# Kernel tuning notes

Hardware: AMD Instinct MI355X
Metric: run time of the kernel (lower is better)

Reference implementation:

```python
import jax, jax.numpy as jnp
import numpy as np

BOUND = 2.0
MIN_NEAR = 0.05
N_RAYS = 131072   # 512x256 image worth of rays
N_COARSE = 128    # coarse intervals -> bins has N_COARSE+1 edges


def setup_inputs() -> dict:
    key = jax.random.key(0)
    k1, k2, k3 = jax.random.split(key, 3)
    rays_o = jax.random.normal(k1, (N_RAYS, 3), jnp.float32) * 0.5  # origins inside the bound cube
    rays_d = jax.random.normal(k2, (N_RAYS, 3), jnp.float32)
    rays_d = rays_d / jnp.linalg.norm(rays_d, axis=-1, keepdims=True)  # unit directions
    weights = jax.random.uniform(k3, (N_RAYS, N_COARSE), jnp.float32)  # coarse-pass weights
    return {"rays_o": rays_o, "rays_d": rays_d, "weights": weights, "n_importance": 128}


def _near_far_cube(rays_o, rays_d, bound, min_near):
    # AABB slab test, identical to near_far_from_bound(type='cube')
    tmin = (-bound - rays_o) / (rays_d + 1e-15)   # [N,3]
    tmax = (bound - rays_o) / (rays_d + 1e-15)
    near = jnp.max(jnp.minimum(tmin, tmax), axis=-1, keepdims=True)  # [N,1]
    far = jnp.min(jnp.maximum(tmin, tmax), axis=-1, keepdims=True)
    miss = far < near
    near = jnp.where(miss, 1e9, near)
    far = jnp.where(miss, 1e9, far)
    near = jnp.maximum(near, min_near)
    return near, far


def _sample_pdf(bins, weights, n_samples):
    # Inverse-CDF importance sampling (det=True), identical math to sample_pdf.
    weights = weights + 1e-5
    pdf = weights / jnp.sum(weights, axis=-1, keepdims=True)           # [N,T]
    cdf = jnp.cumsum(pdf, axis=-1)
    cdf = jnp.concatenate([jnp.zeros_like(cdf[..., :1]), cdf], axis=-1)  # [N,T+1]
    C = cdf.shape[-1]
    u = jnp.linspace(0.5 / n_samples, 1.0 - 0.5 / n_samples, n_samples, dtype=cdf.dtype)
    u = jnp.broadcast_to(u, cdf.shape[:-1] + (n_samples,))              # [N,S]
    inds = jax.vmap(lambda c, uu: jnp.searchsorted(c, uu, side='right'))(cdf, u)
    below = jnp.maximum(inds - 1, 0)
    above = jnp.minimum(inds, C - 1)
    cdf_b = jnp.take_along_axis(cdf, below, axis=-1)    # [N,S]
    cdf_a = jnp.take_along_axis(cdf, above, axis=-1)
    bins_b = jnp.take_along_axis(bins, below, axis=-1)
    bins_a = jnp.take_along_axis(bins, above, axis=-1)
    denom = cdf_a - cdf_b
    denom = jnp.where(denom < 1e-5, jnp.ones_like(denom), denom)
    t = (u - cdf_b) / denom
    return bins_b + t * (bins_a - bins_b)               # [N,S]


def reference(rays_o, rays_d, weights, n_importance):
    near, far = _near_far_cube(rays_o, rays_d, BOUND, MIN_NEAR)
    # uniform coarse bin edges between near and far (as in the renderer's run())
    t = jnp.linspace(0.0, 1.0, weights.shape[-1] + 1, dtype=rays_o.dtype)
    bins = near + (far - near) * t[None, :]             # [N, T+1]
    return _sample_pdf(bins, weights, n_importance)     # [N, n_importance]
```

## Files before the change

### kernel.cpp

```cpp
#include <hip/hip_runtime.h>

#define BOUNDV 2.0f
#define MIN_NEAR 0.05f
#define TCOARSE 128
#define NIMP 128
#define INV128 0.0078125f
#define INV256 0.00390625f

__device__ __forceinline__ float scan16(float S) {
    int m;
    m = __builtin_amdgcn_update_dpp(0, __float_as_int(S), 0x111, 0xf, 0xf, true);
    S += __int_as_float(m);
    m = __builtin_amdgcn_update_dpp(0, __float_as_int(S), 0x112, 0xf, 0xf, true);
    S += __int_as_float(m);
    m = __builtin_amdgcn_update_dpp(0, __float_as_int(S), 0x114, 0xf, 0xf, true);
    S += __int_as_float(m);
    m = __builtin_amdgcn_update_dpp(0, __float_as_int(S), 0x118, 0xf, 0xf, true);
    S += __int_as_float(m);
    return S;
}

__global__ __launch_bounds__(256) void nerf_sample_pdf_kernel(
    const float* __restrict__ rays_o,
    const float* __restrict__ rays_d,
    const float* __restrict__ weights,
    float* __restrict__ out,
    int n_rays)
{
    __shared__ float stg[4][512];

    const int tid  = threadIdx.x;
    const int lane = tid & 63;
    const int wv   = tid >> 6;
    const int grp  = (tid >> 4) & 3;
    const int l16  = tid & 15;
    const int ray  = blockIdx.x * 16 + (tid >> 4);

    if (ray < n_rays) {
        const float* ro = rays_o + (size_t)ray * 3;
        const float* rd = rays_d + (size_t)ray * 3;
        float o0 = ro[0], o1 = ro[1], o2 = ro[2];
        float e0 = rd[0], e1 = rd[1], e2 = rd[2];

        const float* wp = weights + (size_t)ray * TCOARSE + 8 * l16;
        float4 wa = *reinterpret_cast<const float4*>(wp);
        float4 wb = *reinterpret_cast<const float4*>(wp + 4);

        float nr = -1e30f, fr = 1e30f;
        {
            float o[3] = {o0, o1, o2};
            float e[3] = {e0, e1, e2};
            #pragma unroll
            for (int c = 0; c < 3; ++c) {
                float dd = e[c] + 1e-15f;
                float r  = __builtin_amdgcn_rcpf(dd);
                float t0 = (-BOUNDV - o[c]) * r;
                float t1 = ( BOUNDV - o[c]) * r;
                nr = fmaxf(nr, fminf(t0, t1));
                fr = fminf(fr, fmaxf(t0, t1));
            }
        }
        if (fr < nr) { nr = 1e9f; fr = 1e9f; }
        nr = fmaxf(nr, MIN_NEAR);
        float near = nr;
        float bw   = (fr - nr) * INV128;

        float w[8], q[8], invw[8];
        w[0] = wa.x + 1e-5f; w[1] = wa.y + 1e-5f;
        w[2] = wa.z + 1e-5f; w[3] = wa.w + 1e-5f;
        w[4] = wb.x + 1e-5f; w[5] = wb.y + 1e-5f;
        w[6] = wb.z + 1e-5f; w[7] = wb.w + 1e-5f;
        q[0] = w[0];
        #pragma unroll
        for (int j = 1; j < 8; ++j) q[j] = q[j - 1] + w[j];
        #pragma unroll
        for (int j = 0; j < 8; ++j) invw[j] = __builtin_amdgcn_rcpf(w[j]);

        float S    = scan16(q[7]);
        float excl = __int_as_float(__builtin_amdgcn_update_dpp(
            0, __float_as_int(S), 0x111, 0xf, 0xf, true));
        float total = __int_as_float(
            __builtin_amdgcn_ds_swizzle(__float_as_int(S), 0x1F0));
        float it   = __builtin_amdgcn_rcpf(total);
        float s128 = 128.0f * it;
        float t128 = INV128 * total;
        float t256 = INV256 * total;
        float thr  = 1e-5f * total;
        float slr  = bw * it;

        float sl[8];
        #pragma unroll
        for (int j = 0; j < 8; ++j)
            sl[j] = (w[j] < thr) ? slr : bw * invw[j];

        float* srow = &stg[wv][grp * 128];
        float bb = fmaf(bw, (float)(8 * l16), near);

        float p_prev   = excl;
        float knf_prev = ceilf(fmaf(excl, s128, -0.5f));
        int   k_prev   = (int)knf_prev;

        #pragma unroll
        for (int j = 0; j < 8; ++j) {
            float pj  = (j == 7) ? S : (excl + q[j]);
            float knf = ceilf(fmaf(pj, s128, -0.5f));
            int   kn  = (int)knf;
            int   cnt = kn - k_prev;
            float u1   = fmaf(knf_prev, t128, t256);
            float step = t128 * sl[j];
            float v1   = fmaf(u1 - p_prev, sl[j], bb);
            float* pk  = srow + k_prev;
            if (cnt > 0) pk[0] = v1;
            if (cnt > 1) pk[1] = v1 + step;
            if (cnt > 2) pk[2] = fmaf(2.0f, step, v1);
            if (cnt > 3) pk[3] = fmaf(3.0f, step, v1);
            p_prev = pj; k_prev = kn; knf_prev = knf; bb += bw;
        }
    }

    __builtin_amdgcn_wave_barrier();

    int wbase = blockIdx.x * 16 + wv * 4;
    if (wbase + 4 <= n_rays) {
        const float4* sf = reinterpret_cast<const float4*>(&stg[wv][0]);
        float4 v0 = sf[lane];
        float4 v1 = sf[64 + lane];
        float4* ob4 = reinterpret_cast<float4*>(out + (size_t)wbase * NIMP);
        ob4[lane]      = v0;
        ob4[64 + lane] = v1;
    } else if (wbase < n_rays) {
        const float4* sf = reinterpret_cast<const float4*>(&stg[wv][0]);
        float4* ob4 = reinterpret_cast<float4*>(out + (size_t)wbase * NIMP);
        int rays_left = n_rays - wbase;
        if (lane < rays_left * 32)      ob4[lane]      = sf[lane];
        if (64 + lane < rays_left * 32) ob4[64 + lane] = sf[64 + lane];
    }
}

extern "C" void kernel_launch(void* const* d_in, const int* in_sizes, int n_in,
                              void* d_out, int out_size, void* d_ws, size_t ws_size,
                              hipStream_t stream) {
    const float* rays_o  = (const float*)d_in[0];
    const float* rays_d  = (const float*)d_in[1];
    const float* weights = (const float*)d_in[2];
    float* out = (float*)d_out;

    int n_rays = in_sizes[0] / 3;
    int blocks = (n_rays + 15) / 16;
    hipLaunchKernelGGL(nerf_sample_pdf_kernel, dim3(blocks), dim3(256), 0, stream,
                       rays_o, rays_d, weights, out, n_rays);
}
```

Before: 25.77 us.

## Process four ray batches per wave with double-buffered register prefetch

Each wave now handles 16 rays in four batches of 4 instead of a single batch, and the grid shrinks by a factor of four. Loads for the next batch are issued into a second register set before the current batch is computed and flushed, so memory latency overlaps with compute. The cost is fewer blocks, which means less latency hiding through occupancy across the GPU, plus extra registers to hold two ray batches. Wave barriers around each LDS-staged flush keep the shared staging buffer from being overwritten early.

```diff
diff --git a/kernel.cpp b/kernel.cpp
--- a/kernel.cpp
+++ b/kernel.cpp
@@ -20,6 +20,118 @@
     return S;
 }
 
+struct RayRegs {
+    float o0, o1, o2, e0, e1, e2;
+    float4 wa, wb;
+};
+
+__device__ __forceinline__ void issue_loads(const float* __restrict__ rays_o,
+                                            const float* __restrict__ rays_d,
+                                            const float* __restrict__ weights,
+                                            int ray, int l16, bool valid, RayRegs& R)
+{
+    if (!valid) return;
+    const float* ro = rays_o + (size_t)ray * 3;
+    const float* rd = rays_d + (size_t)ray * 3;
+    R.o0 = ro[0]; R.o1 = ro[1]; R.o2 = ro[2];
+    R.e0 = rd[0]; R.e1 = rd[1]; R.e2 = rd[2];
+    const float* wp = weights + (size_t)ray * TCOARSE + 8 * l16;
+    R.wa = *reinterpret_cast<const float4*>(wp);
+    R.wb = *reinterpret_cast<const float4*>(wp + 4);
+}
+
+__device__ __forceinline__ void compute_scatter(const RayRegs& R, int l16,
+                                                float* __restrict__ srow)
+{
+    float nr = -1e30f, fr = 1e30f;
+    {
+        float o[3] = {R.o0, R.o1, R.o2};
+        float e[3] = {R.e0, R.e1, R.e2};
+        #pragma unroll
+        for (int c = 0; c < 3; ++c) {
+            float dd = e[c] + 1e-15f;
+            float r  = __builtin_amdgcn_rcpf(dd);
+            float t0 = (-BOUNDV - o[c]) * r;
+            float t1 = ( BOUNDV - o[c]) * r;
+            nr = fmaxf(nr, fminf(t0, t1));
+            fr = fminf(fr, fmaxf(t0, t1));
+        }
+    }
+    if (fr < nr) { nr = 1e9f; fr = 1e9f; }
+    nr = fmaxf(nr, MIN_NEAR);
+    float near = nr;
+    float bw   = (fr - nr) * INV128;
+
+    float w[8], q[8], sl[8];
+    w[0] = R.wa.x + 1e-5f; w[1] = R.wa.y + 1e-5f;
+    w[2] = R.wa.z + 1e-5f; w[3] = R.wa.w + 1e-5f;
+    w[4] = R.wb.x + 1e-5f; w[5] = R.wb.y + 1e-5f;
+    w[6] = R.wb.z + 1e-5f; w[7] = R.wb.w + 1e-5f;
+    q[0] = w[0];
+    #pragma unroll
+    for (int j = 1; j < 8; ++j) q[j] = q[j - 1] + w[j];
+    #pragma unroll
+    for (int j = 0; j < 8; ++j) sl[j] = __builtin_amdgcn_rcpf(w[j]);
+
+    float S    = scan16(q[7]);
+    float excl = __int_as_float(__builtin_amdgcn_update_dpp(
+        0, __float_as_int(S), 0x111, 0xf, 0xf, true));
+    float total = __int_as_float(
+        __builtin_amdgcn_ds_swizzle(__float_as_int(S), 0x1F0));
+    float it   = __builtin_amdgcn_rcpf(total);
+    float s128 = 128.0f * it;
+    float t128 = INV128 * total;
+    float t256 = INV256 * total;
+    float thr  = 1e-5f * total;
+    float slr  = bw * it;
+
+    #pragma unroll
+    for (int j = 0; j < 8; ++j)
+        sl[j] = (w[j] < thr) ? slr : bw * sl[j];
+
+    float bb = fmaf(bw, (float)(8 * l16), near);
+    float p_prev   = excl;
+    float knf_prev = ceilf(fmaf(excl, s128, -0.5f));
+    int   k_prev   = (int)knf_prev;
+
+    #pragma unroll
+    for (int j = 0; j < 8; ++j) {
+        float pj  = (j == 7) ? S : (excl + q[j]);
+        float knf = ceilf(fmaf(pj, s128, -0.5f));
+        int   kn  = (int)knf;
+        int   cnt = kn - k_prev;
+        float u1   = fmaf(knf_prev, t128, t256);
+        float step = t128 * sl[j];
+        float v1   = fmaf(u1 - p_prev, sl[j], bb);
+        float* pk  = srow + k_prev;
+        if (cnt > 0) pk[0] = v1;
+        if (cnt > 1) pk[1] = v1 + step;
+        if (cnt > 2) pk[2] = fmaf(2.0f, step, v1);
+        if (cnt > 3) pk[3] = fmaf(3.0f, step, v1);
+        p_prev = pj; k_prev = kn; knf_prev = knf; bb += bw;
+    }
+}
+
+__device__ __forceinline__ void flush_batch(const float* __restrict__ stgw,
+                                            float* __restrict__ out,
+                                            int wbase, int lane, int n_rays)
+{
+    __builtin_amdgcn_wave_barrier();
+    const float4* sf = reinterpret_cast<const float4*>(stgw);
+    float4* ob4 = reinterpret_cast<float4*>(out + (size_t)wbase * NIMP);
+    if (wbase + 4 <= n_rays) {
+        float4 v0 = sf[lane];
+        float4 v1 = sf[64 + lane];
+        ob4[lane]      = v0;
+        ob4[64 + lane] = v1;
+    } else if (wbase < n_rays) {
+        int rays_left = n_rays - wbase;
+        if (lane < rays_left * 32)      ob4[lane]      = sf[lane];
+        if (64 + lane < rays_left * 32) ob4[64 + lane] = sf[64 + lane];
+    }
+    __builtin_amdgcn_wave_barrier();
+}
+
 __global__ __launch_bounds__(256) void nerf_sample_pdf_kernel(
     const float* __restrict__ rays_o,
     const float* __restrict__ rays_d,
@@ -34,107 +146,33 @@
     const int wv   = tid >> 6;
     const int grp  = (tid >> 4) & 3;
     const int l16  = tid & 15;
-    const int ray  = blockIdx.x * 16 + (tid >> 4);
 
-    if (ray < n_rays) {
-        const float* ro = rays_o + (size_t)ray * 3;
-        const float* rd = rays_d + (size_t)ray * 3;
-        float o0 = ro[0], o1 = ro[1], o2 = ro[2];
-        float e0 = rd[0], e1 = rd[1], e2 = rd[2];
+    const int wbase = (blockIdx.x * 4 + wv) * 16;
+    const int r0 = wbase + grp;
+    const int r1 = wbase + 4 + grp;
+    const int r2 = wbase + 8 + grp;
+    const int r3 = wbase + 12 + grp;
 
-        const float* wp = weights + (size_t)ray * TCOARSE + 8 * l16;
-        float4 wa = *reinterpret_cast<const float4*>(wp);
-        float4 wb = *reinterpret_cast<const float4*>(wp + 4);
+    float* srow = &stg[wv][grp * 128];
+    float* stgw = &stg[wv][0];
 
-        float nr = -1e30f, fr = 1e30f;
-        {
-            float o[3] = {o0, o1, o2};
-            float e[3] = {e0, e1, e2};
-            #pragma unroll
-            for (int c = 0; c < 3; ++c) {
-                float dd = e[c] + 1e-15f;
-                float r  = __builtin_amdgcn_rcpf(dd);
-                float t0 = (-BOUNDV - o[c]) * r;
-                float t1 = ( BOUNDV - o[c]) * r;
-                nr = fmaxf(nr, fminf(t0, t1));
-                fr = fminf(fr, fmaxf(t0, t1));
-            }
-        }
-        if (fr < nr) { nr = 1e9f; fr = 1e9f; }
-        nr = fmaxf(nr, MIN_NEAR);
-        float near = nr;
-        float bw   = (fr - nr) * INV128;
+    RayRegs A, B;
+    issue_loads(rays_o, rays_d, weights, r0, l16, r0 < n_rays, A);
+    issue_loads(rays_o, rays_d, weights, r1, l16, r1 < n_rays, B);
 
-        float w[8], q[8], invw[8];
-        w[0] = wa.x + 1e-5f; w[1] = wa.y + 1e-5f;
-        w[2] = wa.z + 1e-5f; w[3] = wa.w + 1e-5f;
-        w[4] = wb.x + 1e-5f; w[5] = wb.y + 1e-5f;
-        w[6] = wb.z + 1e-5f; w[7] = wb.w + 1e-5f;
-        q[0] = w[0];
-        #pragma unroll
-        for (int j = 1; j < 8; ++j) q[j] = q[j - 1] + w[j];
-        #pragma unroll
-        for (int j = 0; j < 8; ++j) invw[j] = __builtin_amdgcn_rcpf(w[j]);
+    if (r0 < n_rays) compute_scatter(A, l16, srow);
+    issue_loads(rays_o, rays_d, weights, r2, l16, r2 < n_rays, A);
+    flush_batch(stgw, out, wbase, lane, n_rays);
 
-        float S    = scan16(q[7]);
-        float excl = __int_as_float(__builtin_amdgcn_update_dpp(
-            0, __float_as_int(S), 0x111, 0xf, 0xf, true));
-        float total = __int_as_float(
-            __builtin_amdgcn_ds_swizzle(__float_as_int(S), 0x1F0));
-        float it   = __builtin_amdgcn_rcpf(total);
-        float s128 = 128.0f * it;
-        float t128 = INV128 * total;
-        float t256 = INV256 * total;
-        float thr  = 1e-5f * total;
-        float slr  = bw * it;
+    if (r1 < n_rays) compute_scatter(B, l16, srow);
+    issue_loads(rays_o, rays_d, weights, r3, l16, r3 < n_rays, B);
+    flush_batch(stgw, out, wbase + 4, lane, n_rays);
 
-        float sl[8];
-        #pragma unroll
-        for (int j = 0; j < 8; ++j)
-            sl[j] = (w[j] < thr) ? slr : bw * invw[j];
+    if (r2 < n_rays) compute_scatter(A, l16, srow);
+    flush_batch(stgw, out, wbase + 8, lane, n_rays);
 
-        float* srow = &stg[wv][grp * 128];
-        float bb = fmaf(bw, (float)(8 * l16), near);
-
-        float p_prev   = excl;
-        float knf_prev = ceilf(fmaf(excl, s128, -0.5f));
-        int   k_prev   = (int)knf_prev;
-
-        #pragma unroll
-        for (int j = 0; j < 8; ++j) {
-            float pj  = (j == 7) ? S : (excl + q[j]);
-            float knf = ceilf(fmaf(pj, s128, -0.5f));
-            int   kn  = (int)knf;
-            int   cnt = kn - k_prev;
-            float u1   = fmaf(knf_prev, t128, t256);
-            float step = t128 * sl[j];
-            float v1   = fmaf(u1 - p_prev, sl[j], bb);
-            float* pk  = srow + k_prev;
-            if (cnt > 0) pk[0] = v1;
-            if (cnt > 1) pk[1] = v1 + step;
-            if (cnt > 2) pk[2] = fmaf(2.0f, step, v1);
-            if (cnt > 3) pk[3] = fmaf(3.0f, step, v1);
-            p_prev = pj; k_prev = kn; knf_prev = knf; bb += bw;
-        }
-    }
-
-    __builtin_amdgcn_wave_barrier();
-
-    int wbase = blockIdx.x * 16 + wv * 4;
-    if (wbase + 4 <= n_rays) {
-        const float4* sf = reinterpret_cast<const float4*>(&stg[wv][0]);
-        float4 v0 = sf[lane];
-        float4 v1 = sf[64 + lane];
-        float4* ob4 = reinterpret_cast<float4*>(out + (size_t)wbase * NIMP);
-        ob4[lane]      = v0;
-        ob4[64 + lane] = v1;
-    } else if (wbase < n_rays) {
-        const float4* sf = reinterpret_cast<const float4*>(&stg[wv][0]);
-        float4* ob4 = reinterpret_cast<float4*>(out + (size_t)wbase * NIMP);
-        int rays_left = n_rays - wbase;
-        if (lane < rays_left * 32)      ob4[lane]      = sf[lane];
-        if (64 + lane < rays_left * 32) ob4[64 + lane] = sf[64 + lane];
-    }
+    if (r3 < n_rays) compute_scatter(B, l16, srow);
+    flush_batch(stgw, out, wbase + 12, lane, n_rays);
 }
 
 extern "C" void kernel_launch(void* const* d_in, const int* in_sizes, int n_in,
@@ -146,7 +184,7 @@
     float* out = (float*)d_out;
 
     int n_rays = in_sizes[0] / 3;
-    int blocks = (n_rays + 15) / 16;
+    int blocks = (n_rays + 63) / 64;
     hipLaunchKernelGGL(nerf_sample_pdf_kernel, dim3(blocks), dim3(256), 0, stream,
                        rays_o, rays_d, weights, out, n_rays);
 }
```

Result: slower. 28.81 us (+11.8%).
